# Kernel tuning notes

Hardware: AMD Instinct MI355X
Metric: run time of the kernel (lower is better)

## Reference

```python
import jax, jax.numpy as jnp
import numpy as np

THRESHOLD = 1.0   # threshold_value
ALPHA = 2.0       # spikingjelly surrogate.ATan default alpha


@jax.custom_vjp
def spike(x):
    # Heaviside forward, ATan surrogate backward
    return (x >= 0.0).astype(x.dtype)

def _spike_fwd(x):
    return spike(x), x

def _spike_bwd(x, g):
    # d/dx [ (1/pi) * atan(pi/2 * alpha * x) + 1/2 ] = (alpha/2) / (1 + (pi/2*alpha*x)^2)
    return (g * (ALPHA / 2.0) / (1.0 + (jnp.pi / 2.0 * ALPHA * x) ** 2),)

spike.defvjp(_spike_fwd, _spike_bwd)


def _if_node(v, inp):
    # IFNode with v_reset=None (soft/residual reset): v += I; s = H(v - th); v -= s*th
    v = v + inp
    s = spike(v - THRESHOLD)
    v = v - s * THRESHOLD
    return v, s


def setup_inputs() -> dict:
    key = jax.random.key(0)
    ks = jax.random.split(key, 7)
    B, T = 1024, 128
    H1, H2, C = 512, 256, 18
    def lin(k, fan_out, fan_in):
        bound = 1.0 / np.sqrt(fan_in)
        kw, kb = jax.random.split(k)
        W = jax.random.uniform(kw, (fan_out, fan_in), jnp.float32, -bound, bound)
        b = jax.random.uniform(kb, (fan_out,), jnp.float32, -bound, bound)
        return W, b
    W1, b1 = lin(ks[0], H1, 1)
    W2, b2 = lin(ks[1], H2, H1)
    W3, b3 = lin(ks[2], C, H2)
    x = jax.random.normal(ks[3], (B, T), jnp.float32)
    return {"x": x, "W1": W1, "b1": b1, "W2": W2, "b2": b2,
            "W3": W3, "b3": b3, "repeat": 1}


def reference(x, W1, b1, W2, b2, W3, b3, repeat):
    B, T = x.shape
    H1, H2, C = W1.shape[0], W2.shape[0], W3.shape[0]

    def step(carry, xt):
        v1, v2, v3, acc = carry
        out = xt[:, None]                       # [B, 1]
        for _ in range(repeat):                  # original code only valid for repeat == 1
            v1, s1 = _if_node(v1, out @ W1.T + b1)   # [B, H1]
            v2, s2 = _if_node(v2, s1 @ W2.T + b2)    # [B, H2]
            v3, s3 = _if_node(v3, s2 @ W3.T + b3)    # [B, C]
            out = s3
        return (v1, v2, v3, acc + out), None

    z = lambda d: jnp.zeros((B, d), x.dtype)
    init = (z(H1), z(H2), z(C), z(C))
    (_, _, _, acc), _ = jax.lax.scan(step, init, x.T)   # scan over T timesteps
    return acc / T
```

## Files before the change

kernel.cpp:

```cpp
#include <hip/hip_runtime.h>
#include <cmath>

#define BB  1024
#define TT  128
#define HH1 512
#define HH2 256
#define CC  18

#define WS_DIG   0ull
#define WS_W3D   524288ull
#define WS_MASK  557056ull
#define WS_MASK2 8945664ull
#define WS_D3    13139968ull

typedef int  v4i  __attribute__((ext_vector_type(4)));
typedef int  v16i __attribute__((ext_vector_type(16)));
typedef unsigned long long ull;

__device__ __forceinline__ v4i expand_bits(unsigned bits) {
  v4i a;
  a.x = (int)((( bits        & 15u) * 0x204081u) & 0x01010101u);
  a.y = (int)((((bits >>  4) & 15u) * 0x204081u) & 0x01010101u);
  a.z = (int)((((bits >>  8) & 15u) * 0x204081u) & 0x01010101u);
  a.w = (int)((((bits >> 12) & 15u) * 0x204081u) & 0x01010101u);
  return a;
}

__global__ __launch_bounds__(256) void prep_weights(const float* __restrict__ W2,
    const float* __restrict__ W3, signed char* __restrict__ dig,
    signed char* __restrict__ w3dig)
{
  const int bid = blockIdx.x, tid = threadIdx.x;
  if (bid < 2048) {
    int i = bid * 256 + tid;
    int j = i & 15, n = (i >> 4) & 31, h = (i >> 9) & 1;
    int s = (i >> 10) & 15, d = (i >> 14) & 3, st = i >> 16;
    int h1 = s * 32 + h * 16 + j;
    int h2 = st * 32 + n;
    float w = W2[h2 * HH1 + h1];
    long long ll = llrint((double)w * 4294967296.0);
    int v = (int)ll;
    signed char d0 = (signed char)(v & 255); v = (v - d0) >> 8;
    signed char d1 = (signed char)(v & 255); v = (v - d1) >> 8;
    signed char d2 = (signed char)(v & 255); v = (v - d2) >> 8;
    signed char d3 = (signed char)v;
    dig[i] = (d == 0) ? d0 : (d == 1) ? d1 : (d == 2) ? d2 : d3;
  } else {
    int i = (bid - 2048) * 256 + tid;
    int j = i & 15, col = (i >> 4) & 31, h = (i >> 9) & 1;
    int c8 = (i >> 10) & 7, d = (i >> 13) & 3;
    int h2 = c8 * 32 + h * 16 + j;
    float w = (col < CC) ? W3[col * HH2 + h2] : 0.0f;
    long long ll = llrint((double)w * 4294967296.0);
    int v = (int)ll;
    signed char d0 = (signed char)(v & 255); v = (v - d0) >> 8;
    signed char d1 = (signed char)(v & 255); v = (v - d1) >> 8;
    signed char d2 = (signed char)(v & 255); v = (v - d2) >> 8;
    signed char d3 = (signed char)v;
    w3dig[i] = (d == 0) ? d0 : (d == 1) ? d1 : (d == 2) ? d2 : d3;
  }
}

__global__ __launch_bounds__(256) void phase_s1(const float* __restrict__ x,
    const float* __restrict__ W1, const float* __restrict__ b1,
    ull* __restrict__ masks)
{
  __shared__ float xrow[TT];
  int row = blockIdx.x, tid = threadIdx.x, wv = tid >> 6, lane = tid & 63;
  for (int i = tid; i < TT; i += 256) xrow[i] = x[row * TT + i];
  const float w1a = W1[tid], w1b = W1[tid + 256];
  const float b1a = b1[tid], b1b = b1[tid + 256];
  float v1a = 0.f, v1b = 0.f;
  __syncthreads();
  for (int t = 0; t < TT; ++t) {
    float xt = xrow[t];
    float iA = __fadd_rn(__fmul_rn(xt, w1a), b1a);
    v1a = __fadd_rn(v1a, iA);
    bool sA = (v1a >= 1.0f);  v1a = sA ? (v1a - 1.0f) : v1a;
    float iB = __fadd_rn(__fmul_rn(xt, w1b), b1b);
    v1b = __fadd_rn(v1b, iB);
    bool sB = (v1b >= 1.0f);  v1b = sB ? (v1b - 1.0f) : v1b;
    ull mA = __ballot(sA);
    ull mB = __ballot(sB);
    if (lane == 0) {
      ull* p = masks + (size_t)row * 1024 + (size_t)(t >> 5) * 256 + (t & 31);
      p[(size_t)wv * 32]       = mA;
      p[(size_t)(4 + wv) * 32] = mB;
    }
  }
}

__global__ __launch_bounds__(512, 2) void phase_gemmscan(
    const signed char* __restrict__ Bd, const ull* __restrict__ masks,
    const float* __restrict__ b2, unsigned* __restrict__ masks2)
{
  __shared__ __align__(16) signed char Bl[65536];

  const int bid = blockIdx.x;
  const int rowgrp = bid & 31, stripe = bid >> 5;
  const int tid = threadIdx.x, lane = tid & 63, wv = tid >> 6;
  const int half = lane >> 5, l31 = lane & 31;

  {
    const uint4* src = (const uint4*)(Bd + (size_t)stripe * 65536);
    uint4* dst = (uint4*)Bl;
#pragma unroll
    for (int i = 0; i < 8; ++i) dst[tid + 512 * i] = src[tid + 512 * i];
  }

  const signed char* bbase = Bl + half * 512 + l31 * 16;
  const float b2r = b2[stripe * 32 + l31];
  const unsigned hsh = half * 16;

  const int tp1 = (l31 & 3) + ((l31 >> 3) << 2) + ((l31 & 4) ? 16 : 0);
  const int tp2 = tp1 ^ 16;

  __syncthreads();

  if (wv & 4) {
    __builtin_amdgcn_s_sleep(15);
    __builtin_amdgcn_s_sleep(15);
  }

  for (int tau = 0; tau < 2; ++tau) {
    const int pr = wv + 8 * tau;
    const int r1 = rowgrp * 32 + 2 * pr;
    const ull* mb1 = masks + (size_t)r1 * 1024;
    const ull* mb2 = mb1 + 1024;
    float v2 = 0.f;

    ull wP[8], wQ[8], wPn[8], wQn[8];
#pragma unroll
    for (int k = 0; k < 8; ++k) {
      wP[k] = mb1[k * 32 + tp1];
      wQ[k] = mb2[k * 32 + tp2];
    }

#pragma unroll
    for (int c = 0; c < 4; ++c) {
      if (c < 3) {
#pragma unroll
        for (int k = 0; k < 8; ++k) {
          wPn[k] = mb1[(c + 1) * 256 + k * 32 + tp1];
          wQn[k] = mb2[(c + 1) * 256 + k * 32 + tp2];
        }
      }

      v16i aP[4], aQ[4];
#pragma unroll
      for (int d = 0; d < 4; ++d) {
        aP[d] = (v16i){0,0,0,0,0,0,0,0,0,0,0,0,0,0,0,0};
        aQ[d] = (v16i){0,0,0,0,0,0,0,0,0,0,0,0,0,0,0,0};
      }
      __builtin_amdgcn_s_setprio(1);
#pragma unroll
      for (int s = 0; s < 16; ++s) {
        v4i q0 = *(const v4i*)(bbase + (0 * 16 + s) * 1024);
        v4i q1 = *(const v4i*)(bbase + (1 * 16 + s) * 1024);
        v4i q2 = *(const v4i*)(bbase + (2 * 16 + s) * 1024);
        v4i q3 = *(const v4i*)(bbase + (3 * 16 + s) * 1024);
        unsigned shift = ((s & 1) << 5) + hsh;
        v4i eP = expand_bits((unsigned)(wP[s >> 1] >> shift) & 0xFFFFu);
        v4i eQ = expand_bits((unsigned)(wQ[s >> 1] >> shift) & 0xFFFFu);
        aP[0] = __builtin_amdgcn_mfma_i32_32x32x32_i8(eP, q0, aP[0], 0, 0, 0);
        aQ[0] = __builtin_amdgcn_mfma_i32_32x32x32_i8(eQ, q0, aQ[0], 0, 0, 0);
        aP[1] = __builtin_amdgcn_mfma_i32_32x32x32_i8(eP, q1, aP[1], 0, 0, 0);
        aQ[1] = __builtin_amdgcn_mfma_i32_32x32x32_i8(eQ, q1, aQ[1], 0, 0, 0);
        aP[2] = __builtin_amdgcn_mfma_i32_32x32x32_i8(eP, q2, aP[2], 0, 0, 0);
        aQ[2] = __builtin_amdgcn_mfma_i32_32x32x32_i8(eQ, q2, aQ[2], 0, 0, 0);
        aP[3] = __builtin_amdgcn_mfma_i32_32x32x32_i8(eP, q3, aP[3], 0, 0, 0);
        aQ[3] = __builtin_amdgcn_mfma_i32_32x32x32_i8(eQ, q3, aQ[3], 0, 0, 0);
      }
      __builtin_amdgcn_s_setprio(0);

      float dP[16], dQ[16];
#pragma unroll
      for (int r = 0; r < 16; ++r) {
        int sloP = aP[0][r] + (aP[1][r] << 8);
        int shiP = aP[2][r] + (aP[3][r] << 8);
        double ssP = fma((double)shiP, 65536.0, (double)sloP);
        dP[r] = (float)(ssP * 0x1p-32);
        int sloQ = aQ[0][r] + (aQ[1][r] << 8);
        int shiQ = aQ[2][r] + (aQ[3][r] << 8);
        double ssQ = fma((double)shiQ, 65536.0, (double)sloQ);
        dQ[r] = (float)(ssQ * 0x1p-32);
      }

      const int tb = c * 32;
#pragma unroll
      for (int r = 0; r < 16; ++r) {
        float val = half ? dQ[r] : dP[r];
        float i2 = __fadd_rn(val, b2r);
        v2 = __fadd_rn(v2, i2);
        bool s2 = (v2 >= 1.0f);  v2 = s2 ? (v2 - 1.0f) : v2;
        ull m = __ballot(s2);
        if (lane == 0)
          masks2[(size_t)r1 * 1024 + (size_t)(tb + r) * 8 + stripe] = (unsigned)m;
        else if (lane == 32)
          masks2[(size_t)(r1 + 1) * 1024 + (size_t)(tb + r) * 8 + stripe]
              = (unsigned)(m >> 32);
      }
      v2 = __shfl_xor(v2, 32);
#pragma unroll
      for (int r = 0; r < 16; ++r) {
        float val = half ? dP[r] : dQ[r];
        float i2 = __fadd_rn(val, b2r);
        v2 = __fadd_rn(v2, i2);
        bool s2 = (v2 >= 1.0f);  v2 = s2 ? (v2 - 1.0f) : v2;
        ull m = __ballot(s2);
        if (lane == 0)
          masks2[(size_t)(r1 + 1) * 1024 + (size_t)(tb + 16 + r) * 8 + stripe]
              = (unsigned)m;
        else if (lane == 32)
          masks2[(size_t)r1 * 1024 + (size_t)(tb + 16 + r) * 8 + stripe]
              = (unsigned)(m >> 32);
      }
      v2 = __shfl_xor(v2, 32);

      if (c < 3) {
#pragma unroll
        for (int k = 0; k < 8; ++k) { wP[k] = wPn[k]; wQ[k] = wQn[k]; }
      }
    }
  }
}

__global__ __launch_bounds__(256) void phase_l3v3(const signed char* __restrict__ W3d,
    const unsigned* __restrict__ masks2, const float* __restrict__ b3,
    float* __restrict__ out)
{
  __shared__ __align__(16) signed char Bl[32768];
  const int bid = blockIdx.x;
  const int tid = threadIdx.x, lane = tid & 63, wv = tid >> 6;
  const int half = lane >> 5, l31 = lane & 31;

  {
    const uint4* src = (const uint4*)W3d;
    uint4* dst = (uint4*)Bl;
#pragma unroll
    for (int i = 0; i < 8; ++i) dst[tid + 256 * i] = src[tid + 256 * i];
  }

  const int row = bid * 4 + wv;
  const unsigned* mrow = masks2 + (size_t)row * (TT * 8);
  const signed char* bbase = Bl + half * 512 + l31 * 16;
  const float b3r = b3[l31 < CC ? l31 : 0];
  const unsigned hsh = half * 16;
  const int tp1 = (l31 & 3) + ((l31 >> 3) << 2) + ((l31 & 4) ? 16 : 0);

  __syncthreads();

  float v3 = 0.f, ac = 0.f;

  for (int c = 0; c < 4; ++c) {
    unsigned w8[8];
    {
      const unsigned* mp = mrow + (size_t)(c * 32 + tp1) * 8;
      *(uint4*)&w8[0] = *(const uint4*)mp;
      *(uint4*)&w8[4] = *(const uint4*)(mp + 4);
    }

    v16i acc[4];
#pragma unroll
    for (int d = 0; d < 4; ++d)
      acc[d] = (v16i){0,0,0,0,0,0,0,0,0,0,0,0,0,0,0,0};

#pragma unroll
    for (int c8 = 0; c8 < 8; ++c8) {
      v4i e = expand_bits((w8[c8] >> hsh) & 0xFFFFu);
#pragma unroll
      for (int d = 0; d < 4; ++d) {
        v4i b = *(const v4i*)(bbase + (d * 8 + c8) * 1024);
        acc[d] = __builtin_amdgcn_mfma_i32_32x32x32_i8(e, b, acc[d], 0, 0, 0);
      }
    }

    float dv[16];
#pragma unroll
    for (int r = 0; r < 16; ++r) {
      int slo = acc[0][r] + (acc[1][r] << 8);
      int shi = acc[2][r] + (acc[3][r] << 8);
      double ss = fma((double)shi, 65536.0, (double)slo);
      dv[r] = (float)(ss * 0x1p-32);
    }

#pragma unroll
    for (int r = 0; r < 16; ++r) {
      float i3 = __fadd_rn(dv[r], b3r);
      float u  = __fadd_rn(v3, i3);
      bool s3  = (u >= 1.0f);
      float uv = s3 ? (u - 1.0f) : u;
      float av = __fadd_rn(ac, s3 ? 1.0f : 0.0f);
      if (!half) { v3 = uv; ac = av; }
    }
    v3 = __shfl_xor(v3, 32); ac = __shfl_xor(ac, 32);
#pragma unroll
    for (int r = 0; r < 16; ++r) {
      float i3 = __fadd_rn(dv[r], b3r);
      float u  = __fadd_rn(v3, i3);
      bool s3  = (u >= 1.0f);
      float uv = s3 ? (u - 1.0f) : u;
      float av = __fadd_rn(ac, s3 ? 1.0f : 0.0f);
      if (half) { v3 = uv; ac = av; }
    }
    v3 = __shfl_xor(v3, 32); ac = __shfl_xor(ac, 32);
  }

  if (!half && l31 < CC)
    out[row * CC + l31] = ac * (1.0f / TT);
}

extern "C" void kernel_launch(void* const* d_in, const int* in_sizes, int n_in,
                              void* d_out, int out_size, void* d_ws, size_t ws_size,
                              hipStream_t stream)
{
  (void)in_sizes; (void)n_in; (void)out_size; (void)ws_size;
  const float* x  = (const float*)d_in[0];
  const float* W1 = (const float*)d_in[1];
  const float* b1 = (const float*)d_in[2];
  const float* W2 = (const float*)d_in[3];
  const float* b2 = (const float*)d_in[4];
  const float* W3 = (const float*)d_in[5];
  const float* b3 = (const float*)d_in[6];
  float* out = (float*)d_out;
  char*  ws  = (char*)d_ws;

  signed char* dig    = (signed char*)(ws + WS_DIG);
  signed char* w3dig  = (signed char*)(ws + WS_W3D);
  ull*         masks  = (ull*)(ws + WS_MASK);
  unsigned*    masks2 = (unsigned*)(ws + WS_MASK2);

  prep_weights<<<2176, 256, 0, stream>>>(W2, W3, dig, w3dig);
  phase_s1<<<1024, 256, 0, stream>>>(x, W1, b1, masks);
  phase_gemmscan<<<256, 512, 0, stream>>>(dig, masks, b2, masks2);
  phase_l3v3<<<256, 256, 0, stream>>>(w3dig, masks2, b3, out);
}
```

Baseline: 185.6 us.

## Merge weight prep with layer-1 scan, transpose masks2 layout, prefetch layer-3 masks

Folds the weight digit prep and the layer-1 spike scan into one launch, removing a kernel boundary. The layer-2 spike masks move to a stripe-major, time-major, row-contiguous layout, so each ballot becomes one 64-bit store covering two rows instead of two 32-bit stores. The layer-3 kernel reads the new layout and prefetches the next chunk of masks while computing the current one. The cost is strided gathers in layer 3 across eight stripe planes, in exchange for fewer and wider stores in the scan kernel.

Measured after the change: 194.2 us. 1.05x slower.

```diff
diff --git a/kernel.cpp b/kernel.cpp
--- a/kernel.cpp
+++ b/kernel.cpp
@@ -26,11 +26,15 @@
   return a;
 }
 
-__global__ __launch_bounds__(256) void prep_weights(const float* __restrict__ W2,
-    const float* __restrict__ W3, signed char* __restrict__ dig,
-    signed char* __restrict__ w3dig)
+__global__ __launch_bounds__(256) void prep_all(const float* __restrict__ W2,
+    const float* __restrict__ W3, const float* __restrict__ x,
+    const float* __restrict__ W1, const float* __restrict__ b1,
+    signed char* __restrict__ dig, signed char* __restrict__ w3dig,
+    ull* __restrict__ masks)
 {
+  __shared__ float xrow[TT];
   const int bid = blockIdx.x, tid = threadIdx.x;
+
   if (bid < 2048) {
     int i = bid * 256 + tid;
     int j = i & 15, n = (i >> 4) & 31, h = (i >> 9) & 1;
@@ -45,7 +49,9 @@
     signed char d2 = (signed char)(v & 255); v = (v - d2) >> 8;
     signed char d3 = (signed char)v;
     dig[i] = (d == 0) ? d0 : (d == 1) ? d1 : (d == 2) ? d2 : d3;
-  } else {
+    return;
+  }
+  if (bid < 2176) {
     int i = (bid - 2048) * 256 + tid;
     int j = i & 15, col = (i >> 4) & 31, h = (i >> 9) & 1;
     int c8 = (i >> 10) & 7, d = (i >> 13) & 3;
@@ -58,15 +64,10 @@
     signed char d2 = (signed char)(v & 255); v = (v - d2) >> 8;
     signed char d3 = (signed char)v;
     w3dig[i] = (d == 0) ? d0 : (d == 1) ? d1 : (d == 2) ? d2 : d3;
-  }
-}
-
-__global__ __launch_bounds__(256) void phase_s1(const float* __restrict__ x,
-    const float* __restrict__ W1, const float* __restrict__ b1,
-    ull* __restrict__ masks)
-{
-  __shared__ float xrow[TT];
-  int row = blockIdx.x, tid = threadIdx.x, wv = tid >> 6, lane = tid & 63;
+    return;
+  }
+
+  const int row = bid - 2176, wv = tid >> 6, lane = tid & 63;
   for (int i = tid; i < TT; i += 256) xrow[i] = x[row * TT + i];
   const float w1a = W1[tid], w1b = W1[tid + 256];
   const float b1a = b1[tid], b1b = b1[tid + 256];
@@ -127,6 +128,7 @@
     const int r1 = rowgrp * 32 + 2 * pr;
     const ull* mb1 = masks + (size_t)r1 * 1024;
     const ull* mb2 = mb1 + 1024;
+    unsigned* m2t = masks2 + (size_t)stripe * (TT * BB);
     float v2 = 0.f;
 
     ull wP[8], wQ[8], wPn[8], wQn[8];
@@ -195,10 +197,7 @@
         bool s2 = (v2 >= 1.0f);  v2 = s2 ? (v2 - 1.0f) : v2;
         ull m = __ballot(s2);
         if (lane == 0)
-          masks2[(size_t)r1 * 1024 + (size_t)(tb + r) * 8 + stripe] = (unsigned)m;
-        else if (lane == 32)
-          masks2[(size_t)(r1 + 1) * 1024 + (size_t)(tb + r) * 8 + stripe]
-              = (unsigned)(m >> 32);
+          *(ull*)(m2t + (size_t)(tb + r) * BB + r1) = m;
       }
       v2 = __shfl_xor(v2, 32);
 #pragma unroll
@@ -209,11 +208,7 @@
         bool s2 = (v2 >= 1.0f);  v2 = s2 ? (v2 - 1.0f) : v2;
         ull m = __ballot(s2);
         if (lane == 0)
-          masks2[(size_t)(r1 + 1) * 1024 + (size_t)(tb + 16 + r) * 8 + stripe]
-              = (unsigned)m;
-        else if (lane == 32)
-          masks2[(size_t)r1 * 1024 + (size_t)(tb + 16 + r) * 8 + stripe]
-              = (unsigned)(m >> 32);
+          *(ull*)(m2t + (size_t)(tb + 16 + r) * BB + r1) = (m >> 32) | (m << 32);
       }
       v2 = __shfl_xor(v2, 32);
 
@@ -242,22 +237,24 @@
   }
 
   const int row = bid * 4 + wv;
-  const unsigned* mrow = masks2 + (size_t)row * (TT * 8);
   const signed char* bbase = Bl + half * 512 + l31 * 16;
   const float b3r = b3[l31 < CC ? l31 : 0];
   const unsigned hsh = half * 16;
   const int tp1 = (l31 & 3) + ((l31 >> 3) << 2) + ((l31 & 4) ? 16 : 0);
+  const unsigned* g0 = masks2 + (size_t)tp1 * BB + row;
+
+  float v3 = 0.f, ac = 0.f;
+  unsigned w8[8], w8n[8];
+#pragma unroll
+  for (int k = 0; k < 8; ++k) w8[k] = g0[(size_t)k * (TT * BB)];
 
   __syncthreads();
 
-  float v3 = 0.f, ac = 0.f;
-
   for (int c = 0; c < 4; ++c) {
-    unsigned w8[8];
-    {
-      const unsigned* mp = mrow + (size_t)(c * 32 + tp1) * 8;
-      *(uint4*)&w8[0] = *(const uint4*)mp;
-      *(uint4*)&w8[4] = *(const uint4*)(mp + 4);
+    if (c < 3) {
+      const unsigned* gn = g0 + (size_t)(c + 1) * 32 * BB;
+#pragma unroll
+      for (int k = 0; k < 8; ++k) w8n[k] = gn[(size_t)k * (TT * BB)];
     }
 
     v16i acc[4];
@@ -304,6 +301,11 @@
       if (half) { v3 = uv; ac = av; }
     }
     v3 = __shfl_xor(v3, 32); ac = __shfl_xor(ac, 32);
+
+    if (c < 3) {
+#pragma unroll
+      for (int k = 0; k < 8; ++k) w8[k] = w8n[k];
+    }
   }
 
   if (!half && l31 < CC)
@@ -330,8 +332,7 @@
   ull*         masks  = (ull*)(ws + WS_MASK);
   unsigned*    masks2 = (unsigned*)(ws + WS_MASK2);
 
-  prep_weights<<<2176, 256, 0, stream>>>(W2, W3, dig, w3dig);
-  phase_s1<<<1024, 256, 0, stream>>>(x, W1, b1, masks);
+  prep_all<<<3200, 256, 0, stream>>>(W2, W3, x, W1, b1, dig, w3dig, masks);
   phase_gemmscan<<<256, 512, 0, stream>>>(dig, masks, b2, masks2);
   phase_l3v3<<<256, 256, 0, stream>>>(w3dig, masks2, b3, out);
 }
```
